# Performance work log

Hardware: AMD Instinct MI355X
Metric: run time of the kernel (lower is better)

## Reference

```python
import jax, jax.numpy as jnp
import numpy as np

BITS = 4
GROUP = 128
IN_F = 4096
OUT_F = 4096
MAXQ = (1 << BITS) - 1  # 15
PACK = 32 // BITS       # 8 values per int32


def setup_inputs() -> dict:
    key = jax.random.key(0)
    k1, k2, k3, k4, k5 = jax.random.split(key, 5)
    x = jax.random.normal(k1, (4, 2048, IN_F), dtype=jnp.float32)
    qweight = jax.random.randint(k2, (IN_F // 32 * BITS, OUT_F), 0, 2147483647, dtype=jnp.int32)
    qzeros = jax.random.randint(k3, (IN_F // GROUP, OUT_F // 32 * BITS), 0, 2147483647, dtype=jnp.int32)
    scales = jax.random.uniform(k4, (IN_F // GROUP, OUT_F), dtype=jnp.float32, minval=0.001, maxval=0.01)
    bias = jax.random.normal(k5, (OUT_F,), dtype=jnp.float32) * 0.01
    return {"x": x, "qweight": qweight, "qzeros": qzeros, "scales": scales, "bias": bias}


def _dequant(qweight, qzeros, scales):
    shifts = jnp.arange(0, 32, BITS, dtype=jnp.int32)  # [PACK]
    # zeros: [n_groups, out//PACK, PACK] -> [n_groups, 1, OUT_F]; +1 per GPTQ convention
    zeros = ((qzeros[:, :, None] >> shifts[None, None, :]) & MAXQ) + 1
    zeros = zeros.reshape(-1, 1, OUT_F).astype(scales.dtype)
    # weight: [rows, PACK, OUT_F] -> [n_groups, GROUP, OUT_F]
    w = (qweight[:, None, :] >> shifts[None, :, None]) & MAXQ
    w = w.reshape(-1, GROUP, OUT_F).astype(scales.dtype)
    W = scales[:, None, :] * (w - zeros)
    return W.reshape(IN_F, OUT_F)


def reference(x, qweight, qzeros, scales, bias):
    W = _dequant(qweight, qzeros, scales)          # [IN_F, OUT_F]
    out_shape = x.shape[:-1] + (OUT_F,)
    out = x.reshape(-1, IN_F) @ W                  # [B*S, OUT_F]
    out = out + bias
    return out.reshape(out_shape)
```

## Files before the change

kernel.cpp:

```cpp
#include <hip/hip_runtime.h>
#include <hip/hip_bf16.h>

#define IN_F 4096
#define OUT_F 4096
#define M_ROWS 8192
#define GROUP 128

#define BM 128
#define BN 128
#define BK 32
#define KT_TILES (IN_F / 32)


typedef __attribute__((ext_vector_type(8))) short short8;
typedef __attribute__((ext_vector_type(4))) float floatx4;

__device__ __forceinline__ unsigned short f2bf(float f) {
    unsigned int u = __builtin_bit_cast(unsigned int, f);
    u += 0x7fffu + ((u >> 16) & 1u);
    return (unsigned short)(u >> 16);
}

__device__ __forceinline__ void load_lds16(const unsigned short* g, unsigned short* l) {
    __builtin_amdgcn_global_load_lds(
        (const __attribute__((address_space(1))) void*)g,
        (__attribute__((address_space(3))) void*)l,
        16, 0, 0);
}

__global__ __launch_bounds__(256) void convert_x_kernel(const float* __restrict__ x,
                                                        unsigned short* __restrict__ xb) {
    __shared__ unsigned short tile[16 * 256];

    const int t  = threadIdx.x;
    const int m0 = blockIdx.y * 16;
    const int k0 = blockIdx.x * 256;

    {
        const int r = t & 15;
        const int c = t >> 4;
        const float4* src = (const float4*)(x + (size_t)(m0 + r) * IN_F + k0 + c * 16);
        float4 f[4];
#pragma unroll
        for (int i = 0; i < 4; ++i) f[i] = src[i];
        const float* fs = (const float*)f;
#pragma unroll
        for (int h = 0; h < 2; ++h) {
            const int kl = c * 16 + h * 8;
            const int kt_l = kl >> 5;
            const int q    = (kl >> 3) & 3;
            union { unsigned short us[8]; uint4 v; } o;
#pragma unroll
            for (int j = 0; j < 8; ++j) o.us[j] = f2bf(fs[h * 8 + j]);
            *(uint4*)&tile[kt_l * 512 + (q * 16 + (t & 15)) * 8] = o.v;
        }
    }

    __syncthreads();

    {
        unsigned short* dst = xb + ((size_t)blockIdx.y * KT_TILES + blockIdx.x * 8) * 512;
        *(uint4*)&dst[t * 8]        = *(const uint4*)&tile[t * 8];
        *(uint4*)&dst[2048 + t * 8] = *(const uint4*)&tile[2048 + t * 8];
    }
}

#define DQ_KP 32
#define DQ_N  64

__global__ __launch_bounds__(256) void dequant_kernel(const int* __restrict__ qw,
                                                      const int* __restrict__ qz,
                                                      const float* __restrict__ sc,
                                                      unsigned short* __restrict__ wt) {
    __shared__ unsigned short tile[4 * 8 * 512];

    const int t   = threadIdx.x;
    const int kp0 = blockIdx.x * DQ_KP;
    const int n0  = blockIdx.y * DQ_N;

    {
        const int kp_l = t >> 3;
        const int nq   = t & 7;
        const int kp   = kp0 + kp_l;
        const int g    = kp >> 4;
        const int nb   = n0 + nq * 8;

        const uint4 q0 = *(const uint4*)&qw[(size_t)kp * OUT_F + nb];
        const uint4 q1 = *(const uint4*)&qw[(size_t)kp * OUT_F + nb + 4];
        const unsigned zq = (unsigned)qz[g * (OUT_F / 8) + (nb >> 3)];
        const float4 s0 = *(const float4*)&sc[(size_t)g * OUT_F + nb];
        const float4 s1 = *(const float4*)&sc[(size_t)g * OUT_F + nb + 4];

        unsigned qv[8] = {q0.x, q0.y, q0.z, q0.w, q1.x, q1.y, q1.z, q1.w};
        float    sv[8] = {s0.x, s0.y, s0.z, s0.w, s1.x, s1.y, s1.z, s1.w};

        const int kt_l  = kp_l >> 2;
        const int q_out = kp_l & 3;
        const int tn_l  = nq >> 1;

#pragma unroll
        for (int c = 0; c < 8; ++c) {
            const unsigned q = qv[c];
            const float zero = (float)(((zq >> (4 * c)) & 15u) + 1u);
            const float s = sv[c];
            const int r = (nq * 8 + c) & 15;
            union { unsigned short us[8]; uint4 v; } o;
#pragma unroll
            for (int j = 0; j < 8; ++j) {
                const float w = (float)((q >> (4 * j)) & 15u);
                o.us[j] = f2bf(s * (w - zero));
            }
            *(uint4*)&tile[(tn_l * 8 + kt_l) * 512 + (q_out * 16 + r) * 8] = o.v;
        }
    }

    __syncthreads();

    {
        const int tn0 = blockIdx.y * 4;
        const int kt0 = blockIdx.x * 8;
#pragma unroll
        for (int tn_l = 0; tn_l < 4; ++tn_l) {
            unsigned short* dst = wt + ((size_t)(tn0 + tn_l) * KT_TILES + kt0) * 512;
            const unsigned short* srcl = &tile[tn_l * 4096];
            *(uint4*)&dst[t * 8]        = *(const uint4*)&srcl[t * 8];
            *(uint4*)&dst[2048 + t * 8] = *(const uint4*)&srcl[2048 + t * 8];
        }
    }
}

__global__ __launch_bounds__(256) void gemm_kernel(const unsigned short* __restrict__ xb,
                                                   const unsigned short* __restrict__ wt,
                                                   const float* __restrict__ bias,
                                                   float* __restrict__ out) {
    __shared__ unsigned short As[BM * BK];
    __shared__ unsigned short Bs[BN * BK];

    const int tid  = threadIdx.x;
    const int wid  = tid >> 6;
    const int lane = tid & 63;
    const int TM0 = blockIdx.y * 8;
    const int TN0 = blockIdx.x * 8;
    const int wave_m = wid & 1;
    const int wave_n = wid >> 1;

    floatx4 acc[4][4] = {};

    const unsigned short* ga0 = xb + ((size_t)(TM0 + wid + 0) * KT_TILES) * 512 + lane * 8;
    const unsigned short* ga1 = xb + ((size_t)(TM0 + wid + 4) * KT_TILES) * 512 + lane * 8;
    const unsigned short* gb0 = wt + ((size_t)(TN0 + wid + 0) * KT_TILES) * 512 + lane * 8;
    const unsigned short* gb1 = wt + ((size_t)(TN0 + wid + 4) * KT_TILES) * 512 + lane * 8;
    unsigned short* la0 = &As[(wid + 0) * 512];
    unsigned short* la1 = &As[(wid + 4) * 512];
    unsigned short* lb0 = &Bs[(wid + 0) * 512];
    unsigned short* lb1 = &Bs[(wid + 4) * 512];

    const int a_base = wave_m * 4 * 512 + lane * 8;
    const int b_base = wave_n * 4 * 512 + lane * 8;

    for (int kt = 0; kt < KT_TILES; ++kt) {
        __syncthreads();
        load_lds16(ga0 + kt * 512, la0);
        load_lds16(ga1 + kt * 512, la1);
        load_lds16(gb0 + kt * 512, lb0);
        load_lds16(gb1 + kt * 512, lb1);
        __syncthreads();

        short8 a[4], b[4];
#pragma unroll
        for (int i = 0; i < 4; ++i)
            a[i] = *(const short8*)&As[a_base + i * 512];
#pragma unroll
        for (int j = 0; j < 4; ++j)
            b[j] = *(const short8*)&Bs[b_base + j * 512];
#pragma unroll
        for (int i = 0; i < 4; ++i)
#pragma unroll
            for (int j = 0; j < 4; ++j)
                acc[i][j] = __builtin_amdgcn_mfma_f32_16x16x32_bf16(a[i], b[j], acc[i][j], 0, 0, 0);
    }

    const int mrow = TM0 * 16 + wave_m * 64 + (lane >> 4) * 4;
    const int ncol = TN0 * 16 + wave_n * 64 + (lane & 15);
#pragma unroll
    for (int j = 0; j < 4; ++j) {
        const int n = ncol + j * 16;
        const float bv = bias[n];
#pragma unroll
        for (int i = 0; i < 4; ++i) {
            const int m = mrow + i * 16;
#pragma unroll
            for (int r = 0; r < 4; ++r)
                out[(size_t)(m + r) * OUT_F + n] = acc[i][j][r] + bv;
        }
    }
}

extern "C" void kernel_launch(void* const* d_in, const int* in_sizes, int n_in,
                              void* d_out, int out_size, void* d_ws, size_t ws_size,
                              hipStream_t stream) {
    const float* x    = (const float*)d_in[0];
    const int*   qw   = (const int*)d_in[1];
    const int*   qz   = (const int*)d_in[2];
    const float* sc   = (const float*)d_in[3];
    const float* bias = (const float*)d_in[4];
    float* out = (float*)d_out;

    unsigned short* xb = (unsigned short*)d_ws;
    unsigned short* wt = xb + (size_t)M_ROWS * IN_F;

    convert_x_kernel<<<dim3(IN_F / 256, M_ROWS / 16), 256, 0, stream>>>(x, xb);
    dequant_kernel<<<dim3(IN_F / 8 / DQ_KP, OUT_F / DQ_N), 256, 0, stream>>>(qw, qz, sc, wt);
    gemm_kernel<<<dim3(OUT_F / BN, M_ROWS / BM), 256, 0, stream>>>(xb, wt, bias, out);
}
```

Before: 483.3 us.

## Rewrite GEMM with 256x256 tiles, triple-buffered async LDS loads and block swizzle

The GEMM kernel moves from 128x128 tiles with 4 waves and a single LDS buffer to 256x256 tiles with 8 waves, each wave computing a 128x64 sub-tile. Global-to-LDS loads go into a 3-stage ring buffer with explicit vmcnt waits, so the next tiles are fetched while the current one is computed. Each tile's MFMAs are split into two halves separated by barriers, and setprio is raised during the MFMA bursts. A block-index swizzle groups neighbouring blocks for L2 reuse. The aim is to hide memory latency and raise arithmetic intensity, at the cost of more registers (128 fp32 accumulators per thread), more LDS and fragile hand-placed waitcnt/barrier ordering.

```diff
diff --git a/kernel.cpp b/kernel.cpp
--- a/kernel.cpp
+++ b/kernel.cpp
@@ -6,9 +6,6 @@
 #define M_ROWS 8192
 #define GROUP 128
 
-#define BM 128
-#define BN 128
-#define BK 32
 #define KT_TILES (IN_F / 32)
 
 
@@ -129,65 +126,116 @@
     }
 }
 
-__global__ __launch_bounds__(256) void gemm_kernel(const unsigned short* __restrict__ xb,
-                                                   const unsigned short* __restrict__ wt,
-                                                   const float* __restrict__ bias,
-                                                   float* __restrict__ out) {
-    __shared__ unsigned short As[BM * BK];
-    __shared__ unsigned short Bs[BN * BK];
+__global__ __launch_bounds__(512, 2) void gemm_kernel(const unsigned short* __restrict__ xb,
+                                                      const unsigned short* __restrict__ wt,
+                                                      const float* __restrict__ bias,
+                                                      float* __restrict__ out) {
+    __shared__ unsigned short As[3 * 16 * 512];
+    __shared__ unsigned short Bs[3 * 16 * 512];
 
     const int tid  = threadIdx.x;
     const int wid  = tid >> 6;
     const int lane = tid & 63;
-    const int TM0 = blockIdx.y * 8;
-    const int TN0 = blockIdx.x * 8;
-    const int wave_m = wid & 1;
-    const int wave_n = wid >> 1;
-
-    floatx4 acc[4][4] = {};
-
-    const unsigned short* ga0 = xb + ((size_t)(TM0 + wid + 0) * KT_TILES) * 512 + lane * 8;
-    const unsigned short* ga1 = xb + ((size_t)(TM0 + wid + 4) * KT_TILES) * 512 + lane * 8;
-    const unsigned short* gb0 = wt + ((size_t)(TN0 + wid + 0) * KT_TILES) * 512 + lane * 8;
-    const unsigned short* gb1 = wt + ((size_t)(TN0 + wid + 4) * KT_TILES) * 512 + lane * 8;
-    unsigned short* la0 = &As[(wid + 0) * 512];
-    unsigned short* la1 = &As[(wid + 4) * 512];
-    unsigned short* lb0 = &Bs[(wid + 0) * 512];
-    unsigned short* lb1 = &Bs[(wid + 4) * 512];
-
-    const int a_base = wave_m * 4 * 512 + lane * 8;
-    const int b_base = wave_n * 4 * 512 + lane * 8;
-
-    for (int kt = 0; kt < KT_TILES; ++kt) {
-        __syncthreads();
-        load_lds16(ga0 + kt * 512, la0);
-        load_lds16(ga1 + kt * 512, la1);
-        load_lds16(gb0 + kt * 512, lb0);
-        load_lds16(gb1 + kt * 512, lb1);
-        __syncthreads();
+
+    const int bid = blockIdx.x;
+    const int swz = (bid & 7) * 64 + (bid >> 3);
+    const int bx  = swz & 15;
+    const int by  = swz >> 4;
+
+    const int wm = wid & 1;
+    const int wn = wid >> 1;
+
+    const int TM0 = by * 16;
+    const int TN0 = bx * 16;
+
+    floatx4 acc[8][4] = {};
+
+    const unsigned short* gA0 = xb + ((size_t)(TM0 + wid)     * KT_TILES) * 512 + lane * 8;
+    const unsigned short* gA1 = xb + ((size_t)(TM0 + 8 + wid) * KT_TILES) * 512 + lane * 8;
+    const unsigned short* gB0 = wt + ((size_t)(TN0 + wid)     * KT_TILES) * 512 + lane * 8;
+    const unsigned short* gB1 = wt + ((size_t)(TN0 + 8 + wid) * KT_TILES) * 512 + lane * 8;
+
+    unsigned short* lA0 = &As[wid * 512];
+    unsigned short* lA1 = &As[(8 + wid) * 512];
+    unsigned short* lB0 = &Bs[wid * 512];
+    unsigned short* lB1 = &Bs[(8 + wid) * 512];
+
+    const unsigned short* aBase = &As[(wm * 8) * 512 + lane * 8];
+    const unsigned short* bBase = &Bs[(wn * 4) * 512 + lane * 8];
+
+#define STAGE_A(buf, s) do { \
+        load_lds16(gA0 + (size_t)(s) * 512, lA0 + (buf) * 8192); \
+        load_lds16(gA1 + (size_t)(s) * 512, lA1 + (buf) * 8192); } while (0)
+#define STAGE_B(buf, s) do { \
+        load_lds16(gB0 + (size_t)(s) * 512, lB0 + (buf) * 8192); \
+        load_lds16(gB1 + (size_t)(s) * 512, lB1 + (buf) * 8192); } while (0)
+
+    STAGE_A(0, 0); STAGE_B(0, 0);
+    STAGE_A(1, 1); STAGE_B(1, 1);
+    asm volatile("s_waitcnt vmcnt(4)" ::: "memory");
+    asm volatile("s_barrier" ::: "memory");
+
+    int cur = 0, pre = 2;
+#pragma unroll 1
+    for (int t = 0; t < 128; ++t) {
+        const unsigned short* ab = aBase + cur * 8192;
+        const unsigned short* bb = bBase + cur * 8192;
 
         short8 a[4], b[4];
-#pragma unroll
-        for (int i = 0; i < 4; ++i)
-            a[i] = *(const short8*)&As[a_base + i * 512];
-#pragma unroll
-        for (int j = 0; j < 4; ++j)
-            b[j] = *(const short8*)&Bs[b_base + j * 512];
+
+#pragma unroll
+        for (int j = 0; j < 4; ++j) b[j] = *(const short8*)(bb + j * 512);
+#pragma unroll
+        for (int i = 0; i < 4; ++i) a[i] = *(const short8*)(ab + i * 512);
+        if (t < 126) { STAGE_A(pre, t + 2); }
+        asm volatile("s_barrier" ::: "memory");
+        asm volatile("s_waitcnt lgkmcnt(0)" ::: "memory");
+        __builtin_amdgcn_sched_barrier(0);
+        __builtin_amdgcn_s_setprio(1);
 #pragma unroll
         for (int i = 0; i < 4; ++i)
 #pragma unroll
             for (int j = 0; j < 4; ++j)
                 acc[i][j] = __builtin_amdgcn_mfma_f32_16x16x32_bf16(a[i], b[j], acc[i][j], 0, 0, 0);
-    }
-
-    const int mrow = TM0 * 16 + wave_m * 64 + (lane >> 4) * 4;
-    const int ncol = TN0 * 16 + wave_n * 64 + (lane & 15);
+        __builtin_amdgcn_s_setprio(0);
+        __builtin_amdgcn_sched_barrier(0);
+        asm volatile("s_barrier" ::: "memory");
+
+#pragma unroll
+        for (int i = 0; i < 4; ++i) a[i] = *(const short8*)(ab + (4 + i) * 512);
+        if (t < 126) {
+            STAGE_B(pre, t + 2);
+            asm volatile("s_waitcnt vmcnt(4)" ::: "memory");
+        } else if (t == 126) {
+            asm volatile("s_waitcnt vmcnt(0)" ::: "memory");
+        }
+        asm volatile("s_barrier" ::: "memory");
+        asm volatile("s_waitcnt lgkmcnt(0)" ::: "memory");
+        __builtin_amdgcn_sched_barrier(0);
+        __builtin_amdgcn_s_setprio(1);
+#pragma unroll
+        for (int i = 0; i < 4; ++i)
+#pragma unroll
+            for (int j = 0; j < 4; ++j)
+                acc[4 + i][j] = __builtin_amdgcn_mfma_f32_16x16x32_bf16(a[i], b[j], acc[4 + i][j], 0, 0, 0);
+        __builtin_amdgcn_s_setprio(0);
+        __builtin_amdgcn_sched_barrier(0);
+        asm volatile("s_barrier" ::: "memory");
+
+        cur = (cur == 2) ? 0 : cur + 1;
+        pre = (pre == 2) ? 0 : pre + 1;
+    }
+#undef STAGE_A
+#undef STAGE_B
+
+    const int mrow = TM0 * 16 + wm * 128 + (lane >> 4) * 4;
+    const int ncol = TN0 * 16 + wn * 64 + (lane & 15);
 #pragma unroll
     for (int j = 0; j < 4; ++j) {
         const int n = ncol + j * 16;
         const float bv = bias[n];
 #pragma unroll
-        for (int i = 0; i < 4; ++i) {
+        for (int i = 0; i < 8; ++i) {
             const int m = mrow + i * 16;
 #pragma unroll
             for (int r = 0; r < 4; ++r)
@@ -211,5 +259,5 @@
 
     convert_x_kernel<<<dim3(IN_F / 256, M_ROWS / 16), 256, 0, stream>>>(x, xb);
     dequant_kernel<<<dim3(IN_F / 8 / DQ_KP, OUT_F / DQ_N), 256, 0, stream>>>(qw, qz, sc, wt);
-    gemm_kernel<<<dim3(OUT_F / BN, M_ROWS / BM), 256, 0, stream>>>(xb, wt, bias, out);
-}
+    gemm_kernel<<<dim3((M_ROWS / 256) * (OUT_F / 256)), 512, 0, stream>>>(xb, wt, bias, out);
+}
```

New measurement: 490.6 us. About the same (+1.5%).

## Switch GEMM to 32x32x16 bf16 MFMA with matching pre-tiled operand layouts

Applied to the files above, without the earlier changes.

Replaces the 16x16x32 MFMA tiling with 32x32x16 MFMA. Each wave now computes a 2x2 grid of 32x32 accumulators. The convert and dequant kernels are rewritten to emit operands in a 32-row by 16-k tile layout that matches the new instruction's lane mapping. The bigger instruction should cut the number of MFMA issues and LDS fragment reads per FLOP, in exchange for a new epilogue row mapping and changed LDS write patterns.

```diff
diff --git a/kernel.cpp b/kernel.cpp
--- a/kernel.cpp
+++ b/kernel.cpp
@@ -6,14 +6,10 @@
 #define M_ROWS 8192
 #define GROUP 128
 
-#define BM 128
-#define BN 128
-#define BK 32
-#define KT_TILES (IN_F / 32)
-
+#define KT16 (IN_F / 16)
 
 typedef __attribute__((ext_vector_type(8))) short short8;
-typedef __attribute__((ext_vector_type(4))) float floatx4;
+typedef __attribute__((ext_vector_type(16))) float floatx16;
 
 __device__ __forceinline__ unsigned short f2bf(float f) {
     unsigned int u = __builtin_bit_cast(unsigned int, f);
@@ -30,15 +26,15 @@
 
 __global__ __launch_bounds__(256) void convert_x_kernel(const float* __restrict__ x,
                                                         unsigned short* __restrict__ xb) {
-    __shared__ unsigned short tile[16 * 256];
+    __shared__ unsigned short tile[32 * 128];
 
     const int t  = threadIdx.x;
-    const int m0 = blockIdx.y * 16;
-    const int k0 = blockIdx.x * 256;
-
-    {
-        const int r = t & 15;
-        const int c = t >> 4;
+    const int m0 = blockIdx.y * 32;
+    const int k0 = blockIdx.x * 128;
+
+    {
+        const int r = t >> 3;
+        const int c = t & 7;
         const float4* src = (const float4*)(x + (size_t)(m0 + r) * IN_F + k0 + c * 16);
         float4 f[4];
 #pragma unroll
@@ -46,37 +42,31 @@
         const float* fs = (const float*)f;
 #pragma unroll
         for (int h = 0; h < 2; ++h) {
-            const int kl = c * 16 + h * 8;
-            const int kt_l = kl >> 5;
-            const int q    = (kl >> 3) & 3;
             union { unsigned short us[8]; uint4 v; } o;
 #pragma unroll
             for (int j = 0; j < 8; ++j) o.us[j] = f2bf(fs[h * 8 + j]);
-            *(uint4*)&tile[kt_l * 512 + (q * 16 + (t & 15)) * 8] = o.v;
+            *(uint4*)&tile[c * 512 + (h * 32 + r) * 8] = o.v;
         }
     }
 
     __syncthreads();
 
     {
-        unsigned short* dst = xb + ((size_t)blockIdx.y * KT_TILES + blockIdx.x * 8) * 512;
+        unsigned short* dst = xb + ((size_t)blockIdx.y * KT16 + blockIdx.x * 8) * 512;
         *(uint4*)&dst[t * 8]        = *(const uint4*)&tile[t * 8];
         *(uint4*)&dst[2048 + t * 8] = *(const uint4*)&tile[2048 + t * 8];
     }
 }
-
-#define DQ_KP 32
-#define DQ_N  64
 
 __global__ __launch_bounds__(256) void dequant_kernel(const int* __restrict__ qw,
                                                       const int* __restrict__ qz,
                                                       const float* __restrict__ sc,
                                                       unsigned short* __restrict__ wt) {
-    __shared__ unsigned short tile[4 * 8 * 512];
+    __shared__ unsigned short tile[2 * 16 * 512];
 
     const int t   = threadIdx.x;
-    const int kp0 = blockIdx.x * DQ_KP;
-    const int n0  = blockIdx.y * DQ_N;
+    const int kp0 = blockIdx.x * 32;
+    const int n0  = blockIdx.y * 64;
 
     {
         const int kp_l = t >> 3;
@@ -94,37 +84,38 @@
         unsigned qv[8] = {q0.x, q0.y, q0.z, q0.w, q1.x, q1.y, q1.z, q1.w};
         float    sv[8] = {s0.x, s0.y, s0.z, s0.w, s1.x, s1.y, s1.z, s1.w};
 
-        const int kt_l  = kp_l >> 2;
-        const int q_out = kp_l & 3;
-        const int tn_l  = nq >> 1;
+        const int kt_l  = kp_l >> 1;
+        const int khalf = kp_l & 1;
+        const int nl    = nq >> 2;
 
 #pragma unroll
         for (int c = 0; c < 8; ++c) {
             const unsigned q = qv[c];
             const float zero = (float)(((zq >> (4 * c)) & 15u) + 1u);
             const float s = sv[c];
-            const int r = (nq * 8 + c) & 15;
+            const int nr = (nq & 3) * 8 + c;
             union { unsigned short us[8]; uint4 v; } o;
 #pragma unroll
             for (int j = 0; j < 8; ++j) {
                 const float w = (float)((q >> (4 * j)) & 15u);
                 o.us[j] = f2bf(s * (w - zero));
             }
-            *(uint4*)&tile[(tn_l * 8 + kt_l) * 512 + (q_out * 16 + r) * 8] = o.v;
+            *(uint4*)&tile[(nl * 16 + kt_l) * 512 + (khalf * 32 + nr) * 8] = o.v;
         }
     }
 
     __syncthreads();
 
     {
-        const int tn0 = blockIdx.y * 4;
-        const int kt0 = blockIdx.x * 8;
-#pragma unroll
-        for (int tn_l = 0; tn_l < 4; ++tn_l) {
-            unsigned short* dst = wt + ((size_t)(tn0 + tn_l) * KT_TILES + kt0) * 512;
-            const unsigned short* srcl = &tile[tn_l * 4096];
-            *(uint4*)&dst[t * 8]        = *(const uint4*)&srcl[t * 8];
-            *(uint4*)&dst[2048 + t * 8] = *(const uint4*)&srcl[2048 + t * 8];
+        const int nb0 = blockIdx.y * 2;
+        const int kt0 = blockIdx.x * 16;
+#pragma unroll
+        for (int band = 0; band < 2; ++band) {
+            unsigned short* dst = wt + ((size_t)(nb0 + band) * KT16 + kt0) * 512;
+            const unsigned short* srcl = &tile[band * 8192];
+#pragma unroll
+            for (int p = 0; p < 4; ++p)
+                *(uint4*)&dst[p * 2048 + t * 8] = *(const uint4*)&srcl[p * 2048 + t * 8];
         }
     }
 }
@@ -133,65 +124,66 @@
                                                    const unsigned short* __restrict__ wt,
                                                    const float* __restrict__ bias,
                                                    float* __restrict__ out) {
-    __shared__ unsigned short As[BM * BK];
-    __shared__ unsigned short Bs[BN * BK];
+    __shared__ unsigned short As[8 * 512];
+    __shared__ unsigned short Bs[8 * 512];
 
     const int tid  = threadIdx.x;
     const int wid  = tid >> 6;
     const int lane = tid & 63;
-    const int TM0 = blockIdx.y * 8;
-    const int TN0 = blockIdx.x * 8;
-    const int wave_m = wid & 1;
-    const int wave_n = wid >> 1;
-
-    floatx4 acc[4][4] = {};
-
-    const unsigned short* ga0 = xb + ((size_t)(TM0 + wid + 0) * KT_TILES) * 512 + lane * 8;
-    const unsigned short* ga1 = xb + ((size_t)(TM0 + wid + 4) * KT_TILES) * 512 + lane * 8;
-    const unsigned short* gb0 = wt + ((size_t)(TN0 + wid + 0) * KT_TILES) * 512 + lane * 8;
-    const unsigned short* gb1 = wt + ((size_t)(TN0 + wid + 4) * KT_TILES) * 512 + lane * 8;
-    unsigned short* la0 = &As[(wid + 0) * 512];
-    unsigned short* la1 = &As[(wid + 4) * 512];
-    unsigned short* lb0 = &Bs[(wid + 0) * 512];
-    unsigned short* lb1 = &Bs[(wid + 4) * 512];
-
-    const int a_base = wave_m * 4 * 512 + lane * 8;
-    const int b_base = wave_n * 4 * 512 + lane * 8;
-
-    for (int kt = 0; kt < KT_TILES; ++kt) {
+    const int bx = blockIdx.x;
+    const int by = blockIdx.y;
+    const int wm = wid & 1;
+    const int wn = wid >> 1;
+
+    floatx16 acc[2][2] = {};
+
+    const unsigned short* gA = xb + ((size_t)(by * 4 + wid) * KT16) * 512 + lane * 8;
+    const unsigned short* gB = wt + ((size_t)(bx * 4 + wid) * KT16) * 512 + lane * 8;
+    unsigned short* lA = &As[wid * 1024];
+    unsigned short* lB = &Bs[wid * 1024];
+
+    const unsigned short* aB = &As[wm * 2048 + lane * 8];
+    const unsigned short* bB = &Bs[wn * 2048 + lane * 8];
+
+    for (int kt = 0; kt < 128; ++kt) {
         __syncthreads();
-        load_lds16(ga0 + kt * 512, la0);
-        load_lds16(ga1 + kt * 512, la1);
-        load_lds16(gb0 + kt * 512, lb0);
-        load_lds16(gb1 + kt * 512, lb1);
+        load_lds16(gA + kt * 1024,       lA);
+        load_lds16(gA + kt * 1024 + 512, lA + 512);
+        load_lds16(gB + kt * 1024,       lB);
+        load_lds16(gB + kt * 1024 + 512, lB + 512);
         __syncthreads();
 
-        short8 a[4], b[4];
-#pragma unroll
-        for (int i = 0; i < 4; ++i)
-            a[i] = *(const short8*)&As[a_base + i * 512];
-#pragma unroll
-        for (int j = 0; j < 4; ++j)
-            b[j] = *(const short8*)&Bs[b_base + j * 512];
-#pragma unroll
-        for (int i = 0; i < 4; ++i)
-#pragma unroll
-            for (int j = 0; j < 4; ++j)
-                acc[i][j] = __builtin_amdgcn_mfma_f32_16x16x32_bf16(a[i], b[j], acc[i][j], 0, 0, 0);
-    }
-
-    const int mrow = TM0 * 16 + wave_m * 64 + (lane >> 4) * 4;
-    const int ncol = TN0 * 16 + wave_n * 64 + (lane & 15);
-#pragma unroll
-    for (int j = 0; j < 4; ++j) {
-        const int n = ncol + j * 16;
+        short8 a[2][2], b[2][2];
+#pragma unroll
+        for (int i = 0; i < 2; ++i)
+#pragma unroll
+            for (int h = 0; h < 2; ++h) {
+                a[i][h] = *(const short8*)(aB + (i * 2 + h) * 512);
+                b[i][h] = *(const short8*)(bB + (i * 2 + h) * 512);
+            }
+#pragma unroll
+        for (int h = 0; h < 2; ++h)
+#pragma unroll
+            for (int i = 0; i < 2; ++i)
+#pragma unroll
+                for (int j = 0; j < 2; ++j)
+                    acc[i][j] = __builtin_amdgcn_mfma_f32_32x32x16_bf16(a[i][h], b[j][h], acc[i][j], 0, 0, 0);
+    }
+
+    const int col  = lane & 31;
+    const int rhi  = 4 * (lane >> 5);
+#pragma unroll
+    for (int j = 0; j < 2; ++j) {
+        const int n = bx * 128 + wn * 64 + j * 32 + col;
         const float bv = bias[n];
 #pragma unroll
-        for (int i = 0; i < 4; ++i) {
-            const int m = mrow + i * 16;
-#pragma unroll
-            for (int r = 0; r < 4; ++r)
-                out[(size_t)(m + r) * OUT_F + n] = acc[i][j][r] + bv;
+        for (int i = 0; i < 2; ++i) {
+            const int m0 = by * 128 + wm * 64 + i * 32 + rhi;
+#pragma unroll
+            for (int r = 0; r < 16; ++r) {
+                const int row = (r & 3) + 8 * (r >> 2);
+                out[(size_t)(m0 + row) * OUT_F + n] = acc[i][j][r] + bv;
+            }
         }
     }
 }
@@ -209,7 +201,7 @@
     unsigned short* xb = (unsigned short*)d_ws;
     unsigned short* wt = xb + (size_t)M_ROWS * IN_F;
 
-    convert_x_kernel<<<dim3(IN_F / 256, M_ROWS / 16), 256, 0, stream>>>(x, xb);
-    dequant_kernel<<<dim3(IN_F / 8 / DQ_KP, OUT_F / DQ_N), 256, 0, stream>>>(qw, qz, sc, wt);
-    gemm_kernel<<<dim3(OUT_F / BN, M_ROWS / BM), 256, 0, stream>>>(xb, wt, bias, out);
-}
+    convert_x_kernel<<<dim3(IN_F / 128, M_ROWS / 32), 256, 0, stream>>>(x, xb);
+    dequant_kernel<<<dim3(IN_F / 8 / 32, OUT_F / 64), 256, 0, stream>>>(qw, qz, sc, wt);
+    gemm_kernel<<<dim3(OUT_F / 128, M_ROWS / 128), 256, 0, stream>>>(xb, wt, bias, out);
+}
```

After: 531.2 us. 9.9% more time.
